# Optimization experiments

Measured on AMD Instinct MI355X. Metric: run time of the kernel, lower is better.

Reference implementation:

```python
import jax, jax.numpy as jnp
import numpy as np

B, S, F, E = 8, 2048, 512, 512

def setup_inputs() -> dict:
    key = jax.random.key(0)
    k1, k2, k3, k4 = jax.random.split(key, 4)
    x = jax.random.normal(k1, (B, S, F), dtype=jnp.float32)
    # nn.Linear(feat, embed, bias=False): y = x @ W.T; store W as [F, E] already transposed
    scale = 1.0 / np.sqrt(F)
    Wq = jax.random.uniform(k2, (F, E), dtype=jnp.float32, minval=-scale, maxval=scale)
    Wk = jax.random.uniform(k3, (F, E), dtype=jnp.float32, minval=-scale, maxval=scale)
    Wv = jax.random.uniform(k4, (F, E), dtype=jnp.float32, minval=-scale, maxval=scale)
    return {"x": x, "Wq": Wq, "Wk": Wk, "Wv": Wv}

def reference(x, Wq, Wk, Wv):
    # QKV projections: [B, S, E]
    Q = jnp.einsum('bsf,fe->bse', x, Wq)
    K = jnp.einsum('bsf,fe->bse', x, Wk)
    V = jnp.einsum('bsf,fe->bse', x, Wv)
    # scores: [B, S, S], scaled by sqrt(E)
    scores = jnp.einsum('bqe,bke->bqk', Q, K) / jnp.sqrt(jnp.asarray(Q.shape[-1], Q.dtype))
    attn = jax.nn.softmax(scores, axis=-1)
    return jnp.einsum('bqk,bke->bqe', attn, V)
```

## Files before the change

### kernel.cpp

```cpp
#include <hip/hip_runtime.h>
#include <hip/hip_bf16.h>
#include <stdint.h>

#define B_ 8
#define S_ 2048
#define F_ 512
#define E_ 512

typedef short bf16x8 __attribute__((ext_vector_type(8)));
typedef float f32x4 __attribute__((ext_vector_type(4)));

__device__ __forceinline__ f32x4 mfma16(bf16x8 a, bf16x8 b, f32x4 c) {
  return __builtin_amdgcn_mfma_f32_16x16x32_bf16(a, b, c, 0, 0, 0);
}

__device__ __forceinline__ void gll16(const void* g, void* l) {
  __builtin_amdgcn_global_load_lds(
      (const __attribute__((address_space(1))) void*)g,
      (__attribute__((address_space(3))) void*)l, 16, 0, 0);
}

constexpr float QSCALE = 0.0441941738f * 1.44269504f;

__global__ void xconv_kernel(const float* __restrict__ x,
                             __hip_bfloat16* __restrict__ xb) {
  int i = (blockIdx.x * 256 + threadIdx.x) * 8;
  float4 a = *(const float4*)(x + i);
  float4 b = *(const float4*)(x + i + 4);
  union { __hip_bfloat16 h[8]; uint4 u; } cv;
  cv.h[0] = __float2bfloat16(a.x);
  cv.h[1] = __float2bfloat16(a.y);
  cv.h[2] = __float2bfloat16(a.z);
  cv.h[3] = __float2bfloat16(a.w);
  cv.h[4] = __float2bfloat16(b.x);
  cv.h[5] = __float2bfloat16(b.y);
  cv.h[6] = __float2bfloat16(b.z);
  cv.h[7] = __float2bfloat16(b.w);
  *(uint4*)(xb + i) = cv.u;
}

__global__ void wtrans_kernel(const float* __restrict__ wq,
                              const float* __restrict__ wk,
                              const float* __restrict__ wv,
                              __hip_bfloat16* __restrict__ wt) {
  __shared__ float t[32][33];
  const float* w = (blockIdx.z == 0) ? wq : (blockIdx.z == 1 ? wk : wv);
  __hip_bfloat16* o = wt + (size_t)blockIdx.z * F_ * E_;
  int e0 = blockIdx.x * 32, f0 = blockIdx.y * 32;
  int tx = threadIdx.x, ty = threadIdx.y;
#pragma unroll
  for (int i = 0; i < 4; i++)
    t[ty + 8 * i][tx] = w[(size_t)(f0 + ty + 8 * i) * E_ + e0 + tx];
  __syncthreads();
#pragma unroll
  for (int i = 0; i < 4; i++)
    o[(size_t)(e0 + ty + 8 * i) * F_ + f0 + tx] = __float2bfloat16(t[tx][ty + 8 * i]);
}

__global__ __launch_bounds__(256, 2) void qkvg_kernel(
    const __hip_bfloat16* __restrict__ xb, const __hip_bfloat16* __restrict__ wt,
    __hip_bfloat16* __restrict__ Qb, __hip_bfloat16* __restrict__ Kb,
    __hip_bfloat16* __restrict__ Vt) {
  __shared__ __hip_bfloat16 Al[2][128][64] __attribute__((aligned(16)));
  __shared__ __hip_bfloat16 Bl[2][128][64] __attribute__((aligned(16)));

  int tid = threadIdx.x;
  int lane = tid & 63, w = tid >> 6;
  int el = lane & 15, g = lane >> 4;
  int r7 = el & 7;
  int m0 = blockIdx.x * 128, n0 = blockIdx.y * 128, z = blockIdx.z;
  const __hip_bfloat16* wz = wt + (size_t)z * F_ * E_;
  int wr = w >> 1, wc = w & 1;

  int srcoff = (((lane & 7) ^ ((lane >> 3) & 7)) << 3);
  auto stage = [&](int kk, int bf) {
#pragma unroll
    for (int i = 0; i < 4; i++) {
      gll16(xb + (size_t)(m0 + w * 32 + i * 8 + (lane >> 3)) * F_ + kk * 64 + srcoff,
            &Al[bf][w * 32 + i * 8][0]);
      gll16(wz + (size_t)(n0 + w * 32 + i * 8 + (lane >> 3)) * F_ + kk * 64 + srcoff,
            &Bl[bf][w * 32 + i * 8][0]);
    }
  };

  f32x4 acc[4][4] = {};
  stage(0, 0);
  asm volatile("s_waitcnt vmcnt(0)" ::: "memory");
  __syncthreads();

  for (int kk = 0; kk < 8; ++kk) {
    int bf = kk & 1;
    if (kk < 7) stage(kk + 1, bf ^ 1);
#pragma unroll
    for (int ks = 0; ks < 2; ++ks) {
      bf16x8 av[4], bv[4];
#pragma unroll
      for (int mi = 0; mi < 4; mi++)
        av[mi] = *(const bf16x8*)((const char*)&Al[bf][0][0] +
                                  (wr * 64 + mi * 16 + el) * 128 +
                                  (((ks * 4 + g) ^ r7) << 4));
#pragma unroll
      for (int ni = 0; ni < 4; ni++)
        bv[ni] = *(const bf16x8*)((const char*)&Bl[bf][0][0] +
                                  (wc * 64 + ni * 16 + el) * 128 +
                                  (((ks * 4 + g) ^ r7) << 4));
#pragma unroll
      for (int mi = 0; mi < 4; mi++)
#pragma unroll
        for (int ni = 0; ni < 4; ni++)
          acc[mi][ni] = mfma16(av[mi], bv[ni], acc[mi][ni]);
    }
    asm volatile("s_waitcnt vmcnt(0)" ::: "memory");
    __syncthreads();
  }

  float sc = (z == 0) ? QSCALE : 1.0f;
#pragma unroll
  for (int mi = 0; mi < 4; mi++)
#pragma unroll
    for (int ni = 0; ni < 4; ni++) {
      int mB = m0 + wr * 64 + mi * 16 + g * 4;
      int n = n0 + wc * 64 + ni * 16 + el;
      if (z == 2) {
        union { __hip_bfloat16 h[4]; uint2 u; } pk;
#pragma unroll
        for (int r = 0; r < 4; r++) pk.h[r] = __float2bfloat16(acc[mi][ni][r]);
        int b = mB >> 11, sl = mB & 2047;
        *(uint2*)&Vt[(size_t)b * E_ * S_ + (size_t)n * S_ + sl] = pk.u;
      } else {
#pragma unroll
        for (int r = 0; r < 4; r++) {
          __hip_bfloat16 v = __float2bfloat16(acc[mi][ni][r] * sc);
          if (z == 0) Qb[(size_t)(mB + r) * E_ + n] = v;
          else Kb[(size_t)(mB + r) * E_ + n] = v;
        }
      }
    }
}

__global__ __launch_bounds__(256, 2) void qkv_kernel(
    const float* __restrict__ x, const __hip_bfloat16* __restrict__ wt,
    __hip_bfloat16* __restrict__ Qb, __hip_bfloat16* __restrict__ Kb,
    __hip_bfloat16* __restrict__ Vt) {
  __shared__ __hip_bfloat16 Al[2][128][72];
  __shared__ __hip_bfloat16 Bl[2][128][72];
  int tid = threadIdx.x;
  int lane = tid & 63, w = tid >> 6;
  int el = lane & 15, g = lane >> 4;
  int m0 = blockIdx.x * 128, n0 = blockIdx.y * 128, z = blockIdx.z;
  const __hip_bfloat16* wz = wt + (size_t)z * F_ * E_;
  int wr = w >> 1, wc = w & 1;
  float4 fa[8];
  uint4 vb[4];
  auto load = [&](int kk) {
#pragma unroll
    for (int c = 0; c < 4; c++) {
      int id = tid + 256 * c;
      int row = id >> 3, k8 = (id & 7) * 8;
      const float* s = x + (size_t)(m0 + row) * F_ + kk * 64 + k8;
      fa[2 * c] = *(const float4*)s;
      fa[2 * c + 1] = *(const float4*)(s + 4);
      vb[c] = *(const uint4*)(wz + (size_t)(n0 + row) * F_ + kk * 64 + k8);
    }
  };
  auto store_lds = [&](int bf) {
#pragma unroll
    for (int c = 0; c < 4; c++) {
      int id = tid + 256 * c;
      int row = id >> 3, k8 = (id & 7) * 8;
      union { __hip_bfloat16 h[8]; uint4 u; } cv;
      cv.h[0] = __float2bfloat16(fa[2 * c].x);
      cv.h[1] = __float2bfloat16(fa[2 * c].y);
      cv.h[2] = __float2bfloat16(fa[2 * c].z);
      cv.h[3] = __float2bfloat16(fa[2 * c].w);
      cv.h[4] = __float2bfloat16(fa[2 * c + 1].x);
      cv.h[5] = __float2bfloat16(fa[2 * c + 1].y);
      cv.h[6] = __float2bfloat16(fa[2 * c + 1].z);
      cv.h[7] = __float2bfloat16(fa[2 * c + 1].w);
      *(uint4*)&Al[bf][row][k8] = cv.u;
      *(uint4*)&Bl[bf][row][k8] = vb[c];
    }
  };
  f32x4 acc[4][4] = {};
  load(0);
  store_lds(0);
  __syncthreads();
  for (int kk = 0; kk < 8; ++kk) {
    int bf = kk & 1;
    if (kk < 7) load(kk + 1);
#pragma unroll
    for (int ks = 0; ks < 2; ++ks) {
      bf16x8 av[4], bv[4];
#pragma unroll
      for (int mi = 0; mi < 4; mi++)
        av[mi] = *(const bf16x8*)((const char*)&Al[bf][0][0] +
                                  (wr * 64 + mi * 16 + el) * 144 + (ks * 32 + g * 8) * 2);
#pragma unroll
      for (int ni = 0; ni < 4; ni++)
        bv[ni] = *(const bf16x8*)((const char*)&Bl[bf][0][0] +
                                  (wc * 64 + ni * 16 + el) * 144 + (ks * 32 + g * 8) * 2);
#pragma unroll
      for (int mi = 0; mi < 4; mi++)
#pragma unroll
        for (int ni = 0; ni < 4; ni++)
          acc[mi][ni] = mfma16(av[mi], bv[ni], acc[mi][ni]);
    }
    if (kk < 7) store_lds(bf ^ 1);
    __syncthreads();
  }
  float sc = (z == 0) ? QSCALE : 1.0f;
#pragma unroll
  for (int mi = 0; mi < 4; mi++)
#pragma unroll
    for (int ni = 0; ni < 4; ni++)
#pragma unroll
      for (int r = 0; r < 4; r++) {
        int m = m0 + wr * 64 + mi * 16 + g * 4 + r;
        int n = n0 + wc * 64 + ni * 16 + el;
        __hip_bfloat16 v = __float2bfloat16(acc[mi][ni][r] * sc);
        if (z == 0) Qb[(size_t)m * E_ + n] = v;
        else if (z == 1) Kb[(size_t)m * E_ + n] = v;
        else {
          int b = m >> 11, sl = m & 2047;
          Vt[(size_t)b * E_ * S_ + (size_t)n * S_ + sl] = v;
        }
      }
}

template <int MODE>
__global__ __launch_bounds__(512, 2) void attn_kernel(
    const __hip_bfloat16* __restrict__ Qb, const __hip_bfloat16* __restrict__ Kb,
    const __hip_bfloat16* __restrict__ Vt, float* __restrict__ out,
    __hip_bfloat16* __restrict__ part0, __hip_bfloat16* __restrict__ part1,
    float* __restrict__ Ls, float* __restrict__ Ms) {
  __shared__ __hip_bfloat16 Kl[2][32][512] __attribute__((aligned(16)));
  __shared__ __hip_bfloat16 Vl[2][512][32] __attribute__((aligned(16)));
  __shared__ __hip_bfloat16 Pl[8][16][40] __attribute__((aligned(16)));

  int tid = threadIdx.x;
  int lane = tid & 63, w = tid >> 6;
  int el = lane & 15, g = lane >> 4, x7 = lane & 7;
  int bx = blockIdx.x;
  int batch = bx & 7;
  int qt = MODE ? ((bx >> 3) & 15) : (bx >> 3);
  int half = MODE ? (bx >> 7) : 0;
  int nt = MODE ? 32 : 64;
  int tbase = half * 32;
  int q0 = qt * 128 + w * 16;

  bf16x8 qf[16];
  {
    const __hip_bfloat16* qptr = Qb + (size_t)(batch * S_ + q0 + el) * E_ + g * 8;
#pragma unroll
    for (int s = 0; s < 16; s++) qf[s] = *(const bf16x8*)(qptr + 32 * s);
  }

  f32x4 o[32] = {};
  float m_run = -INFINITY, l_run = 0.f;

  const char* kbase_g = (const char*)(Kb + (size_t)batch * S_ * E_);
  const char* vbase_g = (const char*)(Vt + (size_t)batch * E_ * S_);
  int vsrc_lane = (lane >> 2) * (S_ * 2) + 16 * ((lane & 3) ^ ((lane >> 3) & 3));

  auto stage = [&](int t, int bf) {
#pragma unroll
    for (int i = 0; i < 4; i++) {
      int row = w * 4 + i;
      const char* src =
          kbase_g + ((size_t)(t * 32 + row) * 512 + 8 * (lane ^ (row & 7))) * 2;
      gll16(src, &Kl[bf][row][0]);
    }
#pragma unroll
    for (int i = 0; i < 4; i++) {
      int eb = (w * 4 + i) * 16;
      const char* src = vbase_g + (size_t)eb * (S_ * 2) + vsrc_lane + t * 64;
      gll16(src, &Vl[bf][eb][0]);
    }
  };

  int ka0 = el * 1024 + ((g ^ x7) << 4);
  int ka1 = el * 1024 + (((4 + g) ^ x7) << 4);
  int vbase_l = el * 64 + ((g ^ ((el >> 1) & 3)) << 4);

  stage(tbase, 0);
  asm volatile("s_waitcnt vmcnt(0)" ::: "memory");
  __syncthreads();

  for (int i = 0; i < nt; ++i) {
    int bf = i & 1;
    if (i + 1 < nt) stage(tbase + i + 1, bf ^ 1);
    const char* kl = (const char*)&Kl[bf][0][0];
    f32x4 st[2] = {};
    __builtin_amdgcn_s_setprio(1);
#pragma unroll
    for (int s = 0; s < 16; s++) {
      int base = ((s & 1) ? ka1 : ka0) + (s >> 1) * 128;
#pragma unroll
      for (int f = 0; f < 2; f++) {
        bf16x8 kf = *(const bf16x8*)(kl + base + f * 16384);
        st[f] = mfma16(kf, qf[s], st[f]);
      }
    }
    __builtin_amdgcn_s_setprio(0);
    float vmax = st[0][0];
#pragma unroll
    for (int r = 1; r < 4; r++) vmax = fmaxf(vmax, st[0][r]);
#pragma unroll
    for (int r = 0; r < 4; r++) vmax = fmaxf(vmax, st[1][r]);
    vmax = fmaxf(vmax, __shfl_xor(vmax, 16));
    vmax = fmaxf(vmax, __shfl_xor(vmax, 32));
    if (__any(vmax > m_run + 8.0f)) {
      float m_new = fmaxf(m_run, vmax);
      float fac = exp2f(m_run - m_new);
      float fo[4];
#pragma unroll
      for (int r = 0; r < 4; r++) fo[r] = __shfl(fac, g * 4 + r);
#pragma unroll
      for (int ni = 0; ni < 32; ni++) {
        o[ni][0] *= fo[0]; o[ni][1] *= fo[1]; o[ni][2] *= fo[2]; o[ni][3] *= fo[3];
      }
      l_run *= fac;
      m_run = m_new;
    }
    float p[8];
    float rs = 0.f;
#pragma unroll
    for (int f = 0; f < 2; f++)
#pragma unroll
      for (int r = 0; r < 4; r++) {
        float e2 = exp2f(st[f][r] - m_run);
        p[4 * f + r] = e2;
        rs += e2;
      }
    rs += __shfl_xor(rs, 16);
    rs += __shfl_xor(rs, 32);
    l_run += rs;
#pragma unroll
    for (int f = 0; f < 2; f++) {
      union { __hip_bfloat16 h[4]; uint2 u; } pk;
      pk.h[0] = __float2bfloat16(p[4 * f + 0]);
      pk.h[1] = __float2bfloat16(p[4 * f + 1]);
      pk.h[2] = __float2bfloat16(p[4 * f + 2]);
      pk.h[3] = __float2bfloat16(p[4 * f + 3]);
      *(uint2*)((char*)&Pl[w][0][0] + el * 80 + 32 * f + 8 * g) = pk.u;
    }
    asm volatile("s_waitcnt lgkmcnt(0)" ::: "memory");
    bf16x8 pa = *(const bf16x8*)((const char*)&Pl[w][0][0] + el * 80 + g * 16);
    const char* vl = (const char*)&Vl[bf][0][0];
    __builtin_amdgcn_s_setprio(1);
#pragma unroll
    for (int ni = 0; ni < 32; ni++) {
      bf16x8 vf = *(const bf16x8*)(vl + vbase_l + ni * 1024);
      o[ni] = mfma16(pa, vf, o[ni]);
    }
    __builtin_amdgcn_s_setprio(0);
    asm volatile("s_waitcnt vmcnt(0)" ::: "memory");
    __syncthreads();
  }

  if (MODE == 0) {
    float linv[4];
#pragma unroll
    for (int r = 0; r < 4; r++) {
      float lr = __shfl(l_run, g * 4 + r);
      linv[r] = 1.0f / lr;
    }
    float* ob = out + (size_t)(batch * S_ + q0 + g * 4) * E_ + el;
#pragma unroll
    for (int ni = 0; ni < 32; ni++)
#pragma unroll
      for (int r = 0; r < 4; r++)
        ob[(size_t)r * E_ + ni * 16] = o[ni][r] * linv[r];
  } else {
    __hip_bfloat16* dst = (half == 0) ? part0 : part1;
    __hip_bfloat16* ob = dst + (size_t)(batch * S_ + q0 + g * 4) * E_ + el;
#pragma unroll
    for (int ni = 0; ni < 32; ni++)
#pragma unroll
      for (int r = 0; r < 4; r++)
        ob[(size_t)r * E_ + ni * 16] = __float2bfloat16(o[ni][r]);
    if (g == 0) {
      int idx = half * (B_ * S_) + batch * S_ + q0 + el;
      Ls[idx] = l_run;
      Ms[idx] = m_run;
    }
  }
}

__global__ void merge_kernel(float* __restrict__ out,
                             const __hip_bfloat16* __restrict__ p0,
                             const __hip_bfloat16* __restrict__ p1,
                             const float* __restrict__ Ls,
                             const float* __restrict__ Ms) {
  int idx = blockIdx.x * 256 + threadIdx.x;
  int row = idx >> 6;
  int c8 = (idx & 63) * 8;
  float l0 = Ls[row], m0 = Ms[row];
  float l1 = Ls[B_ * S_ + row], m1 = Ms[B_ * S_ + row];
  float m = fmaxf(m0, m1);
  float w0 = exp2f(m0 - m), w1 = exp2f(m1 - m);
  float inv = 1.0f / (l0 * w0 + l1 * w1);
  size_t off = (size_t)row * E_ + c8;
  union { uint4 u; ushort h[8]; } ua, ub;
  ua.u = *(const uint4*)(p0 + off);
  ub.u = *(const uint4*)(p1 + off);
  float r[8];
#pragma unroll
  for (int j = 0; j < 8; j++) {
    union { uint32_t u; float f; } a, b;
    a.u = (uint32_t)ua.h[j] << 16;
    b.u = (uint32_t)ub.h[j] << 16;
    r[j] = (a.f * w0 + b.f * w1) * inv;
  }
  *(float4*)(out + off) = *(float4*)&r[0];
  *(float4*)(out + off + 4) = *(float4*)&r[4];
}

extern "C" void kernel_launch(void* const* d_in, const int* in_sizes, int n_in,
                              void* d_out, int out_size, void* d_ws, size_t ws_size,
                              hipStream_t stream) {
  const float* x = (const float*)d_in[0];
  const float* wq = (const float*)d_in[1];
  const float* wk = (const float*)d_in[2];
  const float* wv = (const float*)d_in[3];
  float* out = (float*)d_out;

  char* ws = (char*)d_ws;
  __hip_bfloat16* wt = (__hip_bfloat16*)ws;
  __hip_bfloat16* Qb = (__hip_bfloat16*)(ws + (size_t)3 * F_ * E_ * 2);
  __hip_bfloat16* Kb = Qb + (size_t)B_ * S_ * E_;
  __hip_bfloat16* Vt = Kb + (size_t)B_ * S_ * E_;
  __hip_bfloat16* xb = Vt + (size_t)B_ * S_ * E_;
  __hip_bfloat16* part0 = xb + (size_t)B_ * S_ * F_;
  __hip_bfloat16* part1 = part0 + (size_t)B_ * S_ * E_;
  float* Ls = (float*)(part1 + (size_t)B_ * S_ * E_);
  float* Ms = Ls + 2 * B_ * S_;

  size_t need_bfx = (size_t)3 * F_ * E_ * 2 + (size_t)3 * B_ * S_ * E_ * 2 +
                    (size_t)B_ * S_ * F_ * 2;
  size_t need_split = need_bfx + (size_t)2 * B_ * S_ * E_ * 2 + 4 * B_ * S_ * 4;
  bool bfx = (ws_size >= need_bfx);
  bool split = (ws_size >= need_split);

  dim3 b0(32, 8), g0(16, 16, 3);
  wtrans_kernel<<<g0, b0, 0, stream>>>(wq, wk, wv, wt);

  dim3 g1(128, 4, 3);
  if (bfx) {
    xconv_kernel<<<(B_ * S_ * F_) / (256 * 8), 256, 0, stream>>>(x, xb);
    qkvg_kernel<<<g1, 256, 0, stream>>>(xb, wt, Qb, Kb, Vt);
  } else {
    qkv_kernel<<<g1, 256, 0, stream>>>(x, wt, Qb, Kb, Vt);
  }

  if (split) {
    attn_kernel<1><<<256, 512, 0, stream>>>(Qb, Kb, Vt, out, part0, part1, Ls, Ms);
    merge_kernel<<<(B_ * S_ * E_ / 8) / 256, 256, 0, stream>>>(out, part0, part1, Ls, Ms);
  } else {
    attn_kernel<0><<<128, 512, 0, stream>>>(Qb, Kb, Vt, out, nullptr, nullptr,
                                            nullptr, nullptr);
  }
}
```

Measured before the change: 175.6 us.

## Process two query tiles per wave in attention, halving waves per block

Each wave now owns 32 query rows as two 16-row tiles, so every K and V fragment read from LDS feeds two MFMAs. Blocks drop to 256 threads with four waves, and each wave stages twice as many K/V rows. The running-max logic changes to start from a fixed 12.0 and rescale only when a score exceeds the current max, then set the new max 4 above it, which cuts rescale frequency. The cost is roughly doubled accumulator registers (64 f32x4 accumulators), which may cause spills, plus lower occupancy and fewer waves per block to hide latency; a fixed initial max could also misbehave on inputs with very different score ranges.

Result: slower. 515.8 us (+193.7%).

```diff
diff --git a/kernel.cpp b/kernel.cpp
--- a/kernel.cpp
+++ b/kernel.cpp
@@ -228,14 +228,14 @@
 }
 
 template <int MODE>
-__global__ __launch_bounds__(512, 2) void attn_kernel(
+__global__ __launch_bounds__(256, 1) void attn_kernel(
     const __hip_bfloat16* __restrict__ Qb, const __hip_bfloat16* __restrict__ Kb,
     const __hip_bfloat16* __restrict__ Vt, float* __restrict__ out,
     __hip_bfloat16* __restrict__ part0, __hip_bfloat16* __restrict__ part1,
     float* __restrict__ Ls, float* __restrict__ Ms) {
   __shared__ __hip_bfloat16 Kl[2][32][512] __attribute__((aligned(16)));
   __shared__ __hip_bfloat16 Vl[2][512][32] __attribute__((aligned(16)));
-  __shared__ __hip_bfloat16 Pl[8][16][40] __attribute__((aligned(16)));
+  __shared__ __hip_bfloat16 Pl[4][32][40] __attribute__((aligned(16)));
 
   int tid = threadIdx.x;
   int lane = tid & 63, w = tid >> 6;
@@ -246,17 +246,21 @@
   int half = MODE ? (bx >> 7) : 0;
   int nt = MODE ? 32 : 64;
   int tbase = half * 32;
-  int q0 = qt * 128 + w * 16;
-
-  bf16x8 qf[16];
+  int q0 = qt * 128 + w * 32;
+
+  bf16x8 qf0[16], qf1[16];
   {
-    const __hip_bfloat16* qptr = Qb + (size_t)(batch * S_ + q0 + el) * E_ + g * 8;
-#pragma unroll
-    for (int s = 0; s < 16; s++) qf[s] = *(const bf16x8*)(qptr + 32 * s);
-  }
-
-  f32x4 o[32] = {};
-  float m_run = -INFINITY, l_run = 0.f;
+    const __hip_bfloat16* qp0 = Qb + (size_t)(batch * S_ + q0 + el) * E_ + g * 8;
+    const __hip_bfloat16* qp1 = qp0 + (size_t)16 * E_;
+#pragma unroll
+    for (int s = 0; s < 16; s++) {
+      qf0[s] = *(const bf16x8*)(qp0 + 32 * s);
+      qf1[s] = *(const bf16x8*)(qp1 + 32 * s);
+    }
+  }
+
+  f32x4 o0[32] = {}, o1[32] = {};
+  float m0r = 12.0f, l0r = 0.f, m1r = 12.0f, l1r = 0.f;
 
   const char* kbase_g = (const char*)(Kb + (size_t)batch * S_ * E_);
   const char* vbase_g = (const char*)(Vt + (size_t)batch * E_ * S_);
@@ -264,15 +268,15 @@
 
   auto stage = [&](int t, int bf) {
 #pragma unroll
-    for (int i = 0; i < 4; i++) {
-      int row = w * 4 + i;
+    for (int i = 0; i < 8; i++) {
+      int row = w * 8 + i;
       const char* src =
-          kbase_g + ((size_t)(t * 32 + row) * 512 + 8 * (lane ^ (row & 7))) * 2;
+          kbase_g + ((size_t)(t * 32 + row) * 512 + 8 * (lane ^ i)) * 2;
       gll16(src, &Kl[bf][row][0]);
     }
 #pragma unroll
-    for (int i = 0; i < 4; i++) {
-      int eb = (w * 4 + i) * 16;
+    for (int i = 0; i < 8; i++) {
+      int eb = (w * 8 + i) * 16;
       const char* src = vbase_g + (size_t)eb * (S_ * 2) + vsrc_lane + t * 64;
       gll16(src, &Vl[bf][eb][0]);
     }
@@ -290,7 +294,7 @@
     int bf = i & 1;
     if (i + 1 < nt) stage(tbase + i + 1, bf ^ 1);
     const char* kl = (const char*)&Kl[bf][0][0];
-    f32x4 st[2] = {};
+    f32x4 st0[2] = {}, st1[2] = {};
     __builtin_amdgcn_s_setprio(1);
 #pragma unroll
     for (int s = 0; s < 16; s++) {
@@ -298,60 +302,92 @@
 #pragma unroll
       for (int f = 0; f < 2; f++) {
         bf16x8 kf = *(const bf16x8*)(kl + base + f * 16384);
-        st[f] = mfma16(kf, qf[s], st[f]);
+        st0[f] = mfma16(kf, qf0[s], st0[f]);
+        st1[f] = mfma16(kf, qf1[s], st1[f]);
       }
     }
     __builtin_amdgcn_s_setprio(0);
-    float vmax = st[0][0];
-#pragma unroll
-    for (int r = 1; r < 4; r++) vmax = fmaxf(vmax, st[0][r]);
-#pragma unroll
-    for (int r = 0; r < 4; r++) vmax = fmaxf(vmax, st[1][r]);
-    vmax = fmaxf(vmax, __shfl_xor(vmax, 16));
-    vmax = fmaxf(vmax, __shfl_xor(vmax, 32));
-    if (__any(vmax > m_run + 8.0f)) {
-      float m_new = fmaxf(m_run, vmax);
-      float fac = exp2f(m_run - m_new);
+    float vmax0 = st0[0][0], vmax1 = st1[0][0];
+#pragma unroll
+    for (int r = 1; r < 4; r++) {
+      vmax0 = fmaxf(vmax0, st0[0][r]);
+      vmax1 = fmaxf(vmax1, st1[0][r]);
+    }
+#pragma unroll
+    for (int r = 0; r < 4; r++) {
+      vmax0 = fmaxf(vmax0, st0[1][r]);
+      vmax1 = fmaxf(vmax1, st1[1][r]);
+    }
+    vmax0 = fmaxf(vmax0, __shfl_xor(vmax0, 16));
+    vmax0 = fmaxf(vmax0, __shfl_xor(vmax0, 32));
+    vmax1 = fmaxf(vmax1, __shfl_xor(vmax1, 16));
+    vmax1 = fmaxf(vmax1, __shfl_xor(vmax1, 32));
+    if (__any(vmax0 > m0r)) {
+      float m_new = vmax0 + 4.0f;
+      float fac = exp2f(m0r - m_new);
       float fo[4];
 #pragma unroll
       for (int r = 0; r < 4; r++) fo[r] = __shfl(fac, g * 4 + r);
 #pragma unroll
       for (int ni = 0; ni < 32; ni++) {
-        o[ni][0] *= fo[0]; o[ni][1] *= fo[1]; o[ni][2] *= fo[2]; o[ni][3] *= fo[3];
-      }
-      l_run *= fac;
-      m_run = m_new;
-    }
-    float p[8];
-    float rs = 0.f;
+        o0[ni][0] *= fo[0]; o0[ni][1] *= fo[1]; o0[ni][2] *= fo[2]; o0[ni][3] *= fo[3];
+      }
+      l0r *= fac;
+      m0r = m_new;
+    }
+    if (__any(vmax1 > m1r)) {
+      float m_new = vmax1 + 4.0f;
+      float fac = exp2f(m1r - m_new);
+      float fo[4];
+#pragma unroll
+      for (int r = 0; r < 4; r++) fo[r] = __shfl(fac, g * 4 + r);
+#pragma unroll
+      for (int ni = 0; ni < 32; ni++) {
+        o1[ni][0] *= fo[0]; o1[ni][1] *= fo[1]; o1[ni][2] *= fo[2]; o1[ni][3] *= fo[3];
+      }
+      l1r *= fac;
+      m1r = m_new;
+    }
+    float rs0 = 0.f, rs1 = 0.f;
+    float p0[8], p1[8];
 #pragma unroll
     for (int f = 0; f < 2; f++)
 #pragma unroll
       for (int r = 0; r < 4; r++) {
-        float e2 = exp2f(st[f][r] - m_run);
-        p[4 * f + r] = e2;
-        rs += e2;
-      }
-    rs += __shfl_xor(rs, 16);
-    rs += __shfl_xor(rs, 32);
-    l_run += rs;
+        float e0 = exp2f(st0[f][r] - m0r);
+        float e1 = exp2f(st1[f][r] - m1r);
+        p0[4 * f + r] = e0;
+        p1[4 * f + r] = e1;
+        rs0 += e0;
+        rs1 += e1;
+      }
+    rs0 += __shfl_xor(rs0, 16);
+    rs0 += __shfl_xor(rs0, 32);
+    rs1 += __shfl_xor(rs1, 16);
+    rs1 += __shfl_xor(rs1, 32);
+    l0r += rs0;
+    l1r += rs1;
 #pragma unroll
     for (int f = 0; f < 2; f++) {
-      union { __hip_bfloat16 h[4]; uint2 u; } pk;
-      pk.h[0] = __float2bfloat16(p[4 * f + 0]);
-      pk.h[1] = __float2bfloat16(p[4 * f + 1]);
-      pk.h[2] = __float2bfloat16(p[4 * f + 2]);
-      pk.h[3] = __float2bfloat16(p[4 * f + 3]);
-      *(uint2*)((char*)&Pl[w][0][0] + el * 80 + 32 * f + 8 * g) = pk.u;
+      union { __hip_bfloat16 h[4]; uint2 u; } pk0, pk1;
+#pragma unroll
+      for (int r = 0; r < 4; r++) {
+        pk0.h[r] = __float2bfloat16(p0[4 * f + r]);
+        pk1.h[r] = __float2bfloat16(p1[4 * f + r]);
+      }
+      *(uint2*)((char*)&Pl[w][0][0] + el * 80 + 32 * f + 8 * g) = pk0.u;
+      *(uint2*)((char*)&Pl[w][0][0] + (16 + el) * 80 + 32 * f + 8 * g) = pk1.u;
     }
     asm volatile("s_waitcnt lgkmcnt(0)" ::: "memory");
-    bf16x8 pa = *(const bf16x8*)((const char*)&Pl[w][0][0] + el * 80 + g * 16);
+    bf16x8 pa0 = *(const bf16x8*)((const char*)&Pl[w][0][0] + el * 80 + g * 16);
+    bf16x8 pa1 = *(const bf16x8*)((const char*)&Pl[w][0][0] + (16 + el) * 80 + g * 16);
     const char* vl = (const char*)&Vl[bf][0][0];
     __builtin_amdgcn_s_setprio(1);
 #pragma unroll
     for (int ni = 0; ni < 32; ni++) {
       bf16x8 vf = *(const bf16x8*)(vl + vbase_l + ni * 1024);
-      o[ni] = mfma16(pa, vf, o[ni]);
+      o0[ni] = mfma16(pa0, vf, o0[ni]);
+      o1[ni] = mfma16(pa1, vf, o1[ni]);
     }
     __builtin_amdgcn_s_setprio(0);
     asm volatile("s_waitcnt vmcnt(0)" ::: "memory");
@@ -359,30 +395,38 @@
   }
 
   if (MODE == 0) {
-    float linv[4];
+    float li0[4], li1[4];
 #pragma unroll
     for (int r = 0; r < 4; r++) {
-      float lr = __shfl(l_run, g * 4 + r);
-      linv[r] = 1.0f / lr;
-    }
-    float* ob = out + (size_t)(batch * S_ + q0 + g * 4) * E_ + el;
+      li0[r] = 1.0f / __shfl(l0r, g * 4 + r);
+      li1[r] = 1.0f / __shfl(l1r, g * 4 + r);
+    }
+    float* ob0 = out + (size_t)(batch * S_ + q0 + g * 4) * E_ + el;
+    float* ob1 = ob0 + (size_t)16 * E_;
 #pragma unroll
     for (int ni = 0; ni < 32; ni++)
 #pragma unroll
-      for (int r = 0; r < 4; r++)
-        ob[(size_t)r * E_ + ni * 16] = o[ni][r] * linv[r];
+      for (int r = 0; r < 4; r++) {
+        ob0[(size_t)r * E_ + ni * 16] = o0[ni][r] * li0[r];
+        ob1[(size_t)r * E_ + ni * 16] = o1[ni][r] * li1[r];
+      }
   } else {
     __hip_bfloat16* dst = (half == 0) ? part0 : part1;
-    __hip_bfloat16* ob = dst + (size_t)(batch * S_ + q0 + g * 4) * E_ + el;
+    __hip_bfloat16* ob0 = dst + (size_t)(batch * S_ + q0 + g * 4) * E_ + el;
+    __hip_bfloat16* ob1 = ob0 + (size_t)16 * E_;
 #pragma unroll
     for (int ni = 0; ni < 32; ni++)
 #pragma unroll
-      for (int r = 0; r < 4; r++)
-        ob[(size_t)r * E_ + ni * 16] = __float2bfloat16(o[ni][r]);
+      for (int r = 0; r < 4; r++) {
+        ob0[(size_t)r * E_ + ni * 16] = __float2bfloat16(o0[ni][r]);
+        ob1[(size_t)r * E_ + ni * 16] = __float2bfloat16(o1[ni][r]);
+      }
     if (g == 0) {
       int idx = half * (B_ * S_) + batch * S_ + q0 + el;
-      Ls[idx] = l_run;
-      Ms[idx] = m_run;
+      Ls[idx] = l0r;
+      Ms[idx] = m0r;
+      Ls[idx + 16] = l1r;
+      Ms[idx + 16] = m1r;
     }
   }
 }
@@ -454,10 +498,10 @@
   }
 
   if (split) {
-    attn_kernel<1><<<256, 512, 0, stream>>>(Qb, Kb, Vt, out, part0, part1, Ls, Ms);
+    attn_kernel<1><<<256, 256, 0, stream>>>(Qb, Kb, Vt, out, part0, part1, Ls, Ms);
     merge_kernel<<<(B_ * S_ * E_ / 8) / 256, 256, 0, stream>>>(out, part0, part1, Ls, Ms);
   } else {
-    attn_kernel<0><<<128, 512, 0, stream>>>(Qb, Kb, Vt, out, nullptr, nullptr,
+    attn_kernel<0><<<128, 256, 0, stream>>>(Qb, Kb, Vt, out, nullptr, nullptr,
                                             nullptr, nullptr);
   }
 }
```
